# Kernel optimization log

Measured on AMD Instinct MI355X. Metric: run time of the kernel, lower is better.

## Reference

```python
import jax, jax.numpy as jnp
import numpy as np

L = 0.05  # lx = ly = lz box half-extent

# 8 box corners [8,3]
_CORNERS = jnp.array([[sx * L, sy * L, sz * L]
                      for sx in (-1.0, 1.0) for sy in (-1.0, 1.0) for sz in (-1.0, 1.0)],
                     dtype=jnp.float32)
# match original ordering: [-,-,-],[-,-,+],[-,+,-],... which the comprehension above yields


def _euler_R(pose):
    """pose: [B,6] -> R [B,3,3], t [B,3] (yaw, pitch, roll convention from source)."""
    yaw, pitch, roll = pose[:, 0], pose[:, 1], pose[:, 2]
    cy, sy = jnp.cos(yaw), jnp.sin(yaw)
    cp, sp = jnp.cos(pitch), jnp.sin(pitch)
    cr, sr = jnp.cos(roll), jnp.sin(roll)
    R = jnp.stack([
        jnp.stack([cy * cp, cy * sp * sr - sy * cr, cy * sp * cr + sy * sr], axis=-1),
        jnp.stack([sy * cp, sy * sp * sr + cy * cr, sy * sp * cr - cy * sr], axis=-1),
        jnp.stack([-sp, cp * sr, cp * cr], axis=-1),
    ], axis=-2)  # [B,3,3]
    t = pose[:, 3:]  # [B,3]
    return R, t


def _transform_corners(pose):
    R, t = _euler_R(pose)
    # [B,8,3] = corners @ R^T + t
    return jnp.einsum('bij,nj->bni', R, _CORNERS) + t[:, None, :]


def setup_inputs() -> dict:
    key = jax.random.key(0)
    k1, k2, k3, k4 = jax.random.split(key, 4)
    B, C = 1048576, 16
    return {
        'pred_pose': jax.random.normal(k1, (B, 6), dtype=jnp.float32),
        'pred_class': jax.random.normal(k2, (B, C), dtype=jnp.float32),
        'target_pose': jax.random.normal(k3, (B, 6), dtype=jnp.float32),
        'target_class': jax.random.normal(k4, (B, C), dtype=jnp.float32),
    }


def reference(pred_pose, pred_class, target_pose, target_class):
    pts_pred = _transform_corners(pred_pose)    # [B,8,3]
    pts_gt = _transform_corners(target_pose)    # [B,8,3]
    # per-sample pose diff: mean over 8 corner L2 norms, then mean over batch
    norms = jnp.linalg.norm(pts_pred - pts_gt, axis=-1)  # [B,8]
    loss_pose = norms.mean(axis=-1).mean()
    class_loss = jnp.mean((pred_class - target_class) ** 2)
    total_loss = loss_pose + class_loss
    return total_loss, loss_pose, class_loss
```

## Files before the change

### kernel.cpp

```cpp
#include <hip/hip_runtime.h>
#include <math.h>

#define CORNER_L 0.05f

typedef float f4 __attribute__((ext_vector_type(4)));

constexpr int THREADS = 256;
constexpr int CBLOCKS = 2048;
constexpr int PBLOCKS = 2048;

__global__ __launch_bounds__(THREADS) void class_mse_kernel(
    const f4* __restrict__ pc4, const f4* __restrict__ tc4,
    float* __restrict__ ws, int n4)
{
    const int tid = threadIdx.x;
    const size_t G = (size_t)CBLOCKS * THREADS;
    float acc = 0.0f;
    for (size_t i = (size_t)blockIdx.x * THREADS + tid; i < (size_t)n4; i += G) {
        f4 p = __builtin_nontemporal_load(pc4 + i);
        f4 t = __builtin_nontemporal_load(tc4 + i);
        f4 d = p - t;
        acc += d.x * d.x + d.y * d.y + d.z * d.z + d.w * d.w;
    }
    #pragma unroll
    for (int off = 32; off > 0; off >>= 1) acc += __shfl_down(acc, off);
    __shared__ float r[4];
    const int lane = tid & 63, wave = tid >> 6;
    if (lane == 0) r[wave] = acc;
    __syncthreads();
    if (tid == 0) ws[blockIdx.x] = r[0] + r[1] + r[2] + r[3];
}

__device__ __forceinline__ float pose_elem(
    float py, float pp_, float pr, float ptx, float pty, float ptz,
    float ty, float tp_, float tr, float ttx, float tty, float ttz)
{
    float sy1 = __sinf(py),  cy1 = __cosf(py);
    float sp1 = __sinf(pp_), cp1 = __cosf(pp_);
    float sr1 = __sinf(pr),  cr1 = __cosf(pr);
    float sy2 = __sinf(ty),  cy2 = __cosf(ty);
    float sp2 = __sinf(tp_), cp2 = __cosf(tp_);
    float sr2 = __sinf(tr),  cr2 = __cosf(tr);

    float a0 = CORNER_L * (cy1 * cp1 - cy2 * cp2);
    float a1 = CORNER_L * ((cy1 * sp1 * sr1 - sy1 * cr1) - (cy2 * sp2 * sr2 - sy2 * cr2));
    float a2 = CORNER_L * ((cy1 * sp1 * cr1 + sy1 * sr1) - (cy2 * sp2 * cr2 + sy2 * sr2));
    float b0 = CORNER_L * (sy1 * cp1 - sy2 * cp2);
    float b1 = CORNER_L * ((sy1 * sp1 * sr1 + cy1 * cr1) - (sy2 * sp2 * sr2 + cy2 * cr2));
    float b2 = CORNER_L * ((sy1 * sp1 * cr1 - cy1 * sr1) - (sy2 * sp2 * cr2 - cy2 * sr2));
    float c0 = CORNER_L * (sp2 - sp1);
    float c1 = CORNER_L * (cp1 * sr1 - cp2 * sr2);
    float c2 = CORNER_L * (cp1 * cr1 - cp2 * cr2);
    float dtx = ptx - ttx;
    float dty = pty - tty;
    float dtz = ptz - ttz;

    float nsum = 0.0f;
    #pragma unroll
    for (int s = 0; s < 8; ++s) {
        float sx = (s & 4) ? 1.0f : -1.0f;
        float sy = (s & 2) ? 1.0f : -1.0f;
        float sz = (s & 1) ? 1.0f : -1.0f;
        float d0 = sx * a0 + sy * a1 + sz * a2 + dtx;
        float d1 = sx * b0 + sy * b1 + sz * b2 + dty;
        float d2 = sx * c0 + sy * c1 + sz * c2 + dtz;
        nsum += __builtin_amdgcn_sqrtf(d0 * d0 + d1 * d1 + d2 * d2);
    }
    return nsum;
}

__global__ __launch_bounds__(THREADS) void pose_kernel(
    const f4* __restrict__ pp4, const f4* __restrict__ tp4,
    float* __restrict__ ws)
{
    const int tid = threadIdx.x;
    const size_t gtid = (size_t)blockIdx.x * THREADS + tid;
    const size_t f = gtid * 3;

    f4 P0 = __builtin_nontemporal_load(pp4 + f);
    f4 P1 = __builtin_nontemporal_load(pp4 + f + 1);
    f4 P2 = __builtin_nontemporal_load(pp4 + f + 2);
    f4 T0 = __builtin_nontemporal_load(tp4 + f);
    f4 T1 = __builtin_nontemporal_load(tp4 + f + 1);
    f4 T2 = __builtin_nontemporal_load(tp4 + f + 2);

    float acc = 0.0f;
    acc += pose_elem(P0.x, P0.y, P0.z, P0.w, P1.x, P1.y,
                     T0.x, T0.y, T0.z, T0.w, T1.x, T1.y);
    acc += pose_elem(P1.z, P1.w, P2.x, P2.y, P2.z, P2.w,
                     T1.z, T1.w, T2.x, T2.y, T2.z, T2.w);

    #pragma unroll
    for (int off = 32; off > 0; off >>= 1) acc += __shfl_down(acc, off);
    __shared__ float r[4];
    const int lane = tid & 63, wave = tid >> 6;
    if (lane == 0) r[wave] = acc;
    __syncthreads();
    if (tid == 0) ws[CBLOCKS + blockIdx.x] = r[0] + r[1] + r[2] + r[3];
}

__global__ __launch_bounds__(THREADS) void pose_loss_finalize(
    const float* __restrict__ ws, float* __restrict__ out,
    float inv_pose, float inv_class)
{
    float c = 0.0f, p = 0.0f;
    for (int k = threadIdx.x; k < CBLOCKS; k += THREADS) c += ws[k];
    for (int k = threadIdx.x; k < PBLOCKS; k += THREADS) p += ws[CBLOCKS + k];
    #pragma unroll
    for (int off = 32; off > 0; off >>= 1) {
        p += __shfl_down(p, off);
        c += __shfl_down(c, off);
    }
    __shared__ float r_p[4], r_c[4];
    const int lane = threadIdx.x & 63, wave = threadIdx.x >> 6;
    if (lane == 0) { r_p[wave] = p; r_c[wave] = c; }
    __syncthreads();
    if (threadIdx.x == 0) {
        float lp = (r_p[0] + r_p[1] + r_p[2] + r_p[3]) * inv_pose;
        float lc = (r_c[0] + r_c[1] + r_c[2] + r_c[3]) * inv_class;
        out[0] = lp + lc;
        out[1] = lp;
        out[2] = lc;
    }
}

extern "C" void kernel_launch(void* const* d_in, const int* in_sizes, int n_in,
                              void* d_out, int out_size, void* d_ws, size_t ws_size,
                              hipStream_t stream) {
    const f4* pred_pose    = (const f4*)d_in[0];
    const f4* pred_class   = (const f4*)d_in[1];
    const f4* target_pose  = (const f4*)d_in[2];
    const f4* target_class = (const f4*)d_in[3];
    float* out = (float*)d_out;
    float* ws  = (float*)d_ws;

    const int B  = in_sizes[0] / 6;
    const int n4 = B * 4;

    class_mse_kernel<<<CBLOCKS, THREADS, 0, stream>>>(pred_class, target_class, ws, n4);
    pose_kernel<<<PBLOCKS, THREADS, 0, stream>>>(pred_pose, target_pose, ws);

    const float inv_pose  = 1.0f / (8.0f  * (float)B);
    const float inv_class = 1.0f / (16.0f * (float)B);
    pose_loss_finalize<<<1, THREADS, 0, stream>>>(ws, out, inv_pose, inv_class);
}
```

Baseline: 180.1 us.

## Fuse class MSE and pose kernels into one interleaved-block launch

```diff
diff --git a/kernel.cpp b/kernel.cpp
--- a/kernel.cpp
+++ b/kernel.cpp
@@ -6,30 +6,11 @@
 typedef float f4 __attribute__((ext_vector_type(4)));
 
 constexpr int THREADS = 256;
-constexpr int CBLOCKS = 2048;
-constexpr int PBLOCKS = 2048;
-
-__global__ __launch_bounds__(THREADS) void class_mse_kernel(
-    const f4* __restrict__ pc4, const f4* __restrict__ tc4,
-    float* __restrict__ ws, int n4)
-{
-    const int tid = threadIdx.x;
-    const size_t G = (size_t)CBLOCKS * THREADS;
-    float acc = 0.0f;
-    for (size_t i = (size_t)blockIdx.x * THREADS + tid; i < (size_t)n4; i += G) {
-        f4 p = __builtin_nontemporal_load(pc4 + i);
-        f4 t = __builtin_nontemporal_load(tc4 + i);
-        f4 d = p - t;
-        acc += d.x * d.x + d.y * d.y + d.z * d.z + d.w * d.w;
-    }
-    #pragma unroll
-    for (int off = 32; off > 0; off >>= 1) acc += __shfl_down(acc, off);
-    __shared__ float r[4];
-    const int lane = tid & 63, wave = tid >> 6;
-    if (lane == 0) r[wave] = acc;
-    __syncthreads();
-    if (tid == 0) ws[blockIdx.x] = r[0] + r[1] + r[2] + r[3];
-}
+constexpr int GROUPS  = 1024;
+constexpr int CQ = 3, PQ = 2;
+constexpr int CBLOCKS = CQ * GROUPS;
+constexpr int PBLOCKS = PQ * GROUPS;
+constexpr int TOTAL_BLOCKS = CBLOCKS + PBLOCKS;
 
 __device__ __forceinline__ float pose_elem(
     float py, float pp_, float pr, float ptx, float pty, float ptz,
@@ -69,34 +50,53 @@
     return nsum;
 }
 
-__global__ __launch_bounds__(THREADS) void pose_kernel(
-    const f4* __restrict__ pp4, const f4* __restrict__ tp4,
-    float* __restrict__ ws)
+__global__ __launch_bounds__(THREADS) void pose_loss_fused(
+    const f4* __restrict__ pp4, const f4* __restrict__ pc4,
+    const f4* __restrict__ tp4, const f4* __restrict__ tc4,
+    float* __restrict__ ws, int n4)
 {
     const int tid = threadIdx.x;
-    const size_t gtid = (size_t)blockIdx.x * THREADS + tid;
-    const size_t f = gtid * 3;
-
-    f4 P0 = __builtin_nontemporal_load(pp4 + f);
-    f4 P1 = __builtin_nontemporal_load(pp4 + f + 1);
-    f4 P2 = __builtin_nontemporal_load(pp4 + f + 2);
-    f4 T0 = __builtin_nontemporal_load(tp4 + f);
-    f4 T1 = __builtin_nontemporal_load(tp4 + f + 1);
-    f4 T2 = __builtin_nontemporal_load(tp4 + f + 2);
+    const int g   = blockIdx.x;
+    const int grp = g / 5;
+    const int r   = g - grp * 5;
 
     float acc = 0.0f;
-    acc += pose_elem(P0.x, P0.y, P0.z, P0.w, P1.x, P1.y,
-                     T0.x, T0.y, T0.z, T0.w, T1.x, T1.y);
-    acc += pose_elem(P1.z, P1.w, P2.x, P2.y, P2.z, P2.w,
-                     T1.z, T1.w, T2.x, T2.y, T2.z, T2.w);
+    int out_idx;
+
+    if (r < CQ) {
+        const int cb = grp * CQ + r;
+        const size_t G = (size_t)CBLOCKS * THREADS;
+        for (size_t i = (size_t)cb * THREADS + tid; i < (size_t)n4; i += G) {
+            f4 p = __builtin_nontemporal_load(pc4 + i);
+            f4 t = __builtin_nontemporal_load(tc4 + i);
+            f4 d = p - t;
+            acc += d.x * d.x + d.y * d.y + d.z * d.z + d.w * d.w;
+        }
+        out_idx = cb;
+    } else {
+        const int pb = grp * PQ + (r - CQ);
+        const size_t gtid = (size_t)pb * THREADS + tid;
+        const size_t f = gtid * 3;
+        f4 P0 = __builtin_nontemporal_load(pp4 + f);
+        f4 P1 = __builtin_nontemporal_load(pp4 + f + 1);
+        f4 P2 = __builtin_nontemporal_load(pp4 + f + 2);
+        f4 T0 = __builtin_nontemporal_load(tp4 + f);
+        f4 T1 = __builtin_nontemporal_load(tp4 + f + 1);
+        f4 T2 = __builtin_nontemporal_load(tp4 + f + 2);
+        acc += pose_elem(P0.x, P0.y, P0.z, P0.w, P1.x, P1.y,
+                         T0.x, T0.y, T0.z, T0.w, T1.x, T1.y);
+        acc += pose_elem(P1.z, P1.w, P2.x, P2.y, P2.z, P2.w,
+                         T1.z, T1.w, T2.x, T2.y, T2.z, T2.w);
+        out_idx = CBLOCKS + pb;
+    }
 
     #pragma unroll
     for (int off = 32; off > 0; off >>= 1) acc += __shfl_down(acc, off);
-    __shared__ float r[4];
+    __shared__ float red[4];
     const int lane = tid & 63, wave = tid >> 6;
-    if (lane == 0) r[wave] = acc;
+    if (lane == 0) red[wave] = acc;
     __syncthreads();
-    if (tid == 0) ws[CBLOCKS + blockIdx.x] = r[0] + r[1] + r[2] + r[3];
+    if (tid == 0) ws[out_idx] = red[0] + red[1] + red[2] + red[3];
 }
 
 __global__ __launch_bounds__(THREADS) void pose_loss_finalize(
@@ -137,8 +137,8 @@
     const int B  = in_sizes[0] / 6;
     const int n4 = B * 4;
 
-    class_mse_kernel<<<CBLOCKS, THREADS, 0, stream>>>(pred_class, target_class, ws, n4);
-    pose_kernel<<<PBLOCKS, THREADS, 0, stream>>>(pred_pose, target_pose, ws);
+    pose_loss_fused<<<TOTAL_BLOCKS, THREADS, 0, stream>>>(
+        pred_pose, pred_class, target_pose, target_class, ws, n4);
 
     const float inv_pose  = 1.0f / (8.0f  * (float)B);
     const float inv_class = 1.0f / (16.0f * (float)B);
```

Result: faster. 174.6 us (-3.1%).
